# Performance work log

Hardware: AMD Instinct MI355X
Metric: run time of the kernel (lower is better)

The kernel has to match this reference:

```python
import jax, jax.numpy as jnp
import numpy as np

B, Hh, Ww = 8, 64, 64
D_MODEL, D_STATE, D_INNER = 96, 16, 192
R, DH, K = 6, 32, 4           # dt_rank, headdim, scan directions
KR = K * R                    # 24 heads
CHUNK = 64
LN_EPS = 1e-5


def setup_inputs() -> dict:
    key = jax.random.key(0)
    ks = jax.random.split(key, 8)
    s = 0.02
    return {
        "x": jax.random.normal(ks[0], (B, Hh, Ww, D_MODEL), jnp.float32),
        "in_proj_w": jax.random.normal(ks[1], (2 * D_INNER, D_MODEL), jnp.float32) * s,
        "conv_w": jax.random.normal(ks[2], (D_INNER, 1, 3, 3), jnp.float32) * s,
        "conv_b": jnp.zeros((D_INNER,), jnp.float32),
        "x_proj_w": jax.random.normal(ks[3], (K, R + 2 * D_STATE, D_INNER), jnp.float32) * s,
        "A_logs": jnp.zeros((K, R), jnp.float32),          # initialize='v2'
        "Ds": jnp.ones((K, R, DH), jnp.float32),
        "dt_bias": 0.1 * jax.random.uniform(ks[4], (K, R), jnp.float32),
        "ln_w": jnp.ones((D_INNER,), jnp.float32),
        "ln_b": jnp.zeros((D_INNER,), jnp.float32),
        "out_proj_w": jax.random.normal(ks[5], (D_MODEL, D_INNER), jnp.float32) * s,
    }


def _dwconv(x, w, b):
    # x: (B,H,W,C); torch weight (C,1,3,3) -> HWIO (3,3,1,C); depthwise conv, SAME pad
    kern = jnp.transpose(w, (2, 3, 1, 0))
    y = jax.lax.conv_general_dilated(
        x, kern, (1, 1), "SAME",
        dimension_numbers=("NHWC", "HWIO", "NHWC"),
        feature_group_count=x.shape[-1])
    return y + b


def _cross_scan(x):
    # x: (B,H,W,C) -> (B,L,4,C): row-major, col-major, and their reverses
    b, h, w, c = x.shape
    x0 = x.reshape(b, h * w, c)
    x1 = jnp.transpose(x, (0, 2, 1, 3)).reshape(b, h * w, c)
    return jnp.stack([x0, x1, x0[:, ::-1], x1[:, ::-1]], axis=2)


def _cross_merge(ys, h, w):
    # ys: (B,L,4,C) -> (B,L,C), inverse of _cross_scan, summed
    b, l, _, c = ys.shape
    y0 = ys[:, :, 0]
    y1 = jnp.transpose(ys[:, :, 1].reshape(b, w, h, c), (0, 2, 1, 3)).reshape(b, l, c)
    y2 = ys[:, ::-1, 2]
    y3 = jnp.transpose(ys[:, ::-1, 3].reshape(b, w, h, c), (0, 2, 1, 3)).reshape(b, l, c)
    return y0 + y1 + y2 + y3


def _chunk_scan(xs, dts, A, Bm, Cm, Dp, dtb):
    # Mamba2-style chunked selective scan.
    # xs: (B,L,KR,DH), dts: (B,L,KR), A: (KR,), Bm/Cm: (B,L,K,N), Dp: (KR,DH), dtb: (KR,)
    bq, l, h, dh = xs.shape
    n = Bm.shape[-1]
    q = CHUNK
    nc = l // q
    dt = jax.nn.softplus(dts + dtb)                       # (B,L,H)
    g = jnp.arange(h) // R                                # head -> group
    xr = xs.reshape(bq, nc, q, h, dh)
    dtr = dt.reshape(bq, nc, q, h)
    Brh = Bm.reshape(bq, nc, q, K, n)[:, :, :, g, :]      # (B,nc,Q,H,N)
    Crh = Cm.reshape(bq, nc, q, K, n)[:, :, :, g, :]
    dA = dtr * A                                          # (B,nc,Q,H), <= 0
    cum = jnp.cumsum(dA, axis=2)
    # intra-chunk attention-like term
    seg = cum[:, :, :, None, :] - cum[:, :, None, :, :]   # (B,nc,Qt,Qs,H)
    mask = jnp.tril(jnp.ones((q, q), bool))[None, None, :, :, None]
    Mw = jnp.where(mask, jnp.exp(seg), 0.0)
    CB = jnp.einsum("bcthn,bcshn->bctsh", Crh, Brh)
    Wt = CB * Mw * dtr[:, :, None, :, :]                  # dt at source step s
    y_intra = jnp.einsum("bctsh,bcshd->bcthd", Wt, xr)
    # per-chunk contribution to state and chunk decay
    decay_end = jnp.exp(cum[:, :, -1:, :] - cum)          # (B,nc,Q,H)
    S_loc = jnp.einsum("bcsh,bcshn,bcshd->bchdn", decay_end * dtr, Brh, xr)
    a_chunk = jnp.exp(cum[:, :, -1, :])                   # (B,nc,H)
    def step(state, inp):
        a, s = inp
        return a[:, :, None, None] * state + s, state     # emit state BEFORE chunk
    init = jnp.zeros((bq, h, dh, n), xs.dtype)
    _, prevs = jax.lax.scan(step, init, (jnp.moveaxis(a_chunk, 1, 0), jnp.moveaxis(S_loc, 1, 0)))
    prev_states = jnp.moveaxis(prevs, 0, 1)               # (B,nc,H,DH,N)
    y_inter = jnp.einsum("bcth,bcthn,bchdn->bcthd", jnp.exp(cum), Crh, prev_states)
    y = y_intra + y_inter + xr * Dp
    return y.reshape(bq, l, h, dh)


def _layernorm(x, w, b):
    mu = jnp.mean(x, -1, keepdims=True)
    var = jnp.mean(jnp.square(x - mu), -1, keepdims=True)
    return (x - mu) * jax.lax.rsqrt(var + LN_EPS) * w + b


def reference(x, in_proj_w, conv_w, conv_b, x_proj_w, A_logs, Ds, dt_bias, ln_w, ln_b, out_proj_w):
    bq, hh, ww, _ = x.shape
    l = hh * ww
    xz = x @ in_proj_w.T                                  # (B,H,W,2*Dinner)
    xh, z = jnp.split(xz, 2, axis=-1)
    z = jax.nn.silu(z)
    xh = jax.nn.silu(_dwconv(xh, conv_w, conv_b))
    xs = _cross_scan(xh)                                  # (B,L,K,Dinner)
    x_dbl = jnp.einsum("blkd,kcd->blkc", xs, x_proj_w)
    dts, Bs, Cs = jnp.split(x_dbl, [R, R + D_STATE], axis=3)
    xs = xs.reshape(bq, l, KR, DH)
    dts = dts.reshape(bq, l, KR)
    A = -jnp.exp(A_logs.reshape(KR))
    Dp = Ds.reshape(KR, DH)
    dtb = dt_bias.reshape(KR)
    ys = _chunk_scan(xs, dts, A, Bs, Cs, Dp, dtb)         # (B,L,KR,DH)
    y = _cross_merge(ys.reshape(bq, l, K, D_INNER), hh, ww)
    y = _layernorm(y, ln_w, ln_b).reshape(bq, hh, ww, D_INNER)
    y = y * z
    return y @ out_proj_w.T
```

## Files before the change

kernel.cpp:

```cpp
#include <hip/hip_runtime.h>
#include <hip/hip_bf16.h>

using bf16 = __hip_bfloat16;
typedef float f32;
typedef __attribute__((ext_vector_type(8))) short bf16x8;
typedef __attribute__((ext_vector_type(4))) float f32x4;
typedef __attribute__((ext_vector_type(4))) unsigned short u16x4;
typedef __attribute__((ext_vector_type(8))) unsigned short u16x8;

static __device__ __forceinline__ f32 siluf(f32 v){ return v / (1.f + __expf(-v)); }
static __device__ __forceinline__ unsigned short f2bf(f32 v){
  __hip_bfloat16 h=__float2bfloat16(v); return *(unsigned short*)&h;
}
static __device__ __forceinline__ f32 bfr2f(unsigned short u){
  unsigned int x=((unsigned int)u)<<16; return __uint_as_float(x);
}

static __device__ __forceinline__ int pos_of(int dir, int p){
  if(dir==0) return p;
  if(dir==1) return ((p&63)<<6) | (p>>6);
  if(dir==2) return 4095-p;
  int q = 4095-p; return ((q&63)<<6) | (q>>6);
}

static __device__ __forceinline__ f32 wave_iscan(f32 v, int lane){
  #pragma unroll
  for(int off=1; off<64; off<<=1){
    f32 u=__shfl_up(v,off,64);
    if(lane>=off) v+=u;
  }
  return v;
}
static __device__ __forceinline__ f32 wave_sscan(f32 v, int lane){
  #pragma unroll
  for(int off=1; off<64; off<<=1){
    f32 u=__shfl_down(v,off,64);
    if(lane<64-off) v+=u;
  }
  return v;
}

__global__ __launch_bounds__(256) void k_wcvt_all(const f32* __restrict__ xpw, const f32* __restrict__ ipw,
                                                  const f32* __restrict__ opw, const f32* __restrict__ dsw,
                                                  unsigned short* __restrict__ Wx, unsigned short* __restrict__ Wi,
                                                  unsigned short* __restrict__ Wo, f32* __restrict__ Dsum){
  const int t=blockIdx.x*256+threadIdx.x;
  if(t<3840){
    const int g=t%24, n=t/24, nt=n>>4, l=n&15;
    const int dir=n/40, cc=n-dir*40;
    u16x8 w={0,0,0,0,0,0,0,0};
    if(cc<38){
      const f32* p=&xpw[(size_t)dir*7296+cc*192+g*8];
      #pragma unroll
      for(int j=0;j<8;j++) w[j]=f2bf(p[j]);
    }
    *(u16x8*)&Wx[((size_t)(nt*24+g)*16+l)*8]=w;
  } else if(t<8448){
    const int i=t-3840, g=i%12, n=i/12, nt=n>>4, l=n&15;
    const f32* p=&ipw[(size_t)n*96+g*8];
    u16x8 w;
    #pragma unroll
    for(int j=0;j<8;j++) w[j]=f2bf(p[j]);
    *(u16x8*)&Wi[((size_t)(nt*12+g)*16+l)*8]=w;
  } else if(t<10752){
    const int i=t-8448, g=i%24, n=i/24, nt=n>>4, l=n&15;
    const f32* p=&opw[(size_t)n*192+g*8];
    u16x8 w;
    #pragma unroll
    for(int j=0;j<8;j++) w[j]=f2bf(p[j]);
    *(u16x8*)&Wo[((size_t)(nt*24+g)*16+l)*8]=w;
  } else if(t<10944){
    const int ch=t-10752;
    Dsum[ch]=dsw[ch]+dsw[192+ch]+dsw[384+ch]+dsw[576+ch];
  }
}

__global__ __launch_bounds__(256) void k_inproj(const f32* __restrict__ x, const unsigned short* __restrict__ Wi,
                                                f32* __restrict__ xh_raw, f32* __restrict__ z){
  __shared__ unsigned short Ald[12*64*8];
  const int m0=blockIdx.x*64, tid=threadIdx.x;
  for(int i=tid;i<768;i+=256){
    int r=i&63, g=i>>6;
    const f32* p=&x[(size_t)(m0+r)*96+g*8];
    float4 v0=*(const float4*)p, v1=*(const float4*)(p+4);
    u16x8 w={f2bf(v0.x),f2bf(v0.y),f2bf(v0.z),f2bf(v0.w),
             f2bf(v1.x),f2bf(v1.y),f2bf(v1.z),f2bf(v1.w)};
    *(u16x8*)&Ald[(size_t)(g*64+r)*8]=w;
  }
  __syncthreads();
  const int wv=tid>>6, lane=tid&63, l15=lane&15, l4=lane>>4;
  f32x4 acc[24];
  #pragma unroll
  for(int nt=0;nt<24;nt++){ f32x4 zz={0.f,0.f,0.f,0.f}; acc[nt]=zz; }
  #pragma unroll
  for(int ks=0;ks<3;ks++){
    const int g=ks*4+l4;
    bf16x8 a=*(const bf16x8*)&Ald[(size_t)(g*64+wv*16+l15)*8];
    #pragma unroll
    for(int nt=0;nt<24;nt++){
      bf16x8 bfr=*(const bf16x8*)&Wi[((size_t)(nt*12+g)*16+l15)*8];
      acc[nt]=__builtin_amdgcn_mfma_f32_16x16x32_bf16(a,bfr,acc[nt],0,0,0);
    }
  }
  const int rowb=m0+wv*16+l4*4;
  #pragma unroll
  for(int nt=0;nt<24;nt++){
    int col=nt*16+l15;
    #pragma unroll
    for(int r=0;r<4;r++){
      int row=rowb+r; f32 v=acc[nt][r];
      if(col<192) xh_raw[(size_t)row*192+col]=v;
      else        z[(size_t)row*192+(col-192)]=siluf(v);
    }
  }
}

__global__ __launch_bounds__(256) void k_conv(const f32* __restrict__ xh_raw, const f32* __restrict__ cw,
                                              const f32* __restrict__ cb, f32* __restrict__ xh){
  __shared__ f32 wsm[192][9];
  __shared__ f32 bsm[192];
  const int tid=threadIdx.x;
  for(int i=tid;i<1728;i+=256) wsm[i/9][i%9]=cw[i];
  for(int i=tid;i<192;i+=256) bsm[i]=cb[i];
  __syncthreads();
  const int idx=blockIdx.x*256+tid;
  const int c4=idx%48, j=(idx/48)&63, ii0=(idx/3072)&63, b=idx/196608;
  const int c0=c4*4;
  f32 acc[4]={bsm[c0],bsm[c0+1],bsm[c0+2],bsm[c0+3]};
  #pragma unroll
  for(int a=0;a<3;a++){
    int ii=ii0+a-1; if(ii<0||ii>63) continue;
    #pragma unroll
    for(int bb=0;bb<3;bb++){
      int jj=j+bb-1; if(jj<0||jj>63) continue;
      float4 v=*(const float4*)&xh_raw[((size_t)(b*4096)+(ii*64+jj))*192 + c0];
      int t=a*3+bb;
      acc[0]+=v.x*wsm[c0][t]; acc[1]+=v.y*wsm[c0+1][t];
      acc[2]+=v.z*wsm[c0+2][t]; acc[3]+=v.w*wsm[c0+3][t];
    }
  }
  float4 o; o.x=siluf(acc[0]); o.y=siluf(acc[1]); o.z=siluf(acc[2]); o.w=siluf(acc[3]);
  ((float4*)xh)[idx]=o;
}

__global__ __launch_bounds__(256) void k_xdbl(const f32* __restrict__ xh, const unsigned short* __restrict__ Wfrag,
                                              const f32* __restrict__ dtb, f32* __restrict__ dt_sp,
                                              f32* __restrict__ Bg, f32* __restrict__ Cg){
  __shared__ unsigned short Ald[24*64*8];
  const int m0=blockIdx.x*64;
  const int tid=threadIdx.x;
  for(int i=tid;i<1536;i+=256){
    int r=i&63, g=i>>6;
    const f32* p=&xh[(size_t)(m0+r)*192 + g*8];
    float4 v0=*(const float4*)p, v1=*(const float4*)(p+4);
    u16x8 w={f2bf(v0.x),f2bf(v0.y),f2bf(v0.z),f2bf(v0.w),
             f2bf(v1.x),f2bf(v1.y),f2bf(v1.z),f2bf(v1.w)};
    *(u16x8*)&Ald[(size_t)(g*64+r)*8]=w;
  }
  __syncthreads();
  const int wv=tid>>6, lane=tid&63, l15=lane&15, l4=lane>>4;
  f32x4 acc[10];
  #pragma unroll
  for(int nt=0;nt<10;nt++){ f32x4 zz={0.f,0.f,0.f,0.f}; acc[nt]=zz; }
  #pragma unroll
  for(int ks=0;ks<6;ks++){
    const int g=ks*4+l4;
    bf16x8 a=*(const bf16x8*)&Ald[(size_t)(g*64 + wv*16 + l15)*8];
    #pragma unroll
    for(int nt=0;nt<10;nt++){
      bf16x8 bfr=*(const bf16x8*)&Wfrag[((size_t)(nt*24+g)*16+l15)*8];
      acc[nt]=__builtin_amdgcn_mfma_f32_16x16x32_bf16(a,bfr,acc[nt],0,0,0);
    }
  }
  const int rowb=m0 + wv*16 + l4*4;
  #pragma unroll
  for(int nt=0;nt<10;nt++){
    int n=nt*16+l15, dir=n/40, cc=n-dir*40;
    if(cc>=38) continue;
    #pragma unroll
    for(int r=0;r<4;r++){
      size_t pix=(size_t)(rowb+r);
      f32 v=acc[nt][r];
      if(cc<6){ f32 xv=v+dtb[dir*6+cc]; dt_sp[pix*24+dir*6+cc]=(xv>20.f)? xv : log1pf(__expf(xv)); }
      else if(cc<22){ Bg[(pix*4+dir)*16+(cc-6)]=v; }
      else          { Cg[(pix*4+dir)*16+(cc-22)]=v; }
    }
  }
}

#define LDK1 72
__global__ __launch_bounds__(384) void k_chunk1(const f32* __restrict__ xh, const f32* __restrict__ Bg,
      const f32* __restrict__ dt_sp, const f32* __restrict__ Alogs, f32* __restrict__ S, f32* __restrict__ ach){
  __shared__ unsigned short Bp[192*LDK1];
  __shared__ unsigned short BtT[16*LDK1];
  __shared__ f32 dtl[64][6], w1l[64][6];
  __shared__ f32 e63[6];
  const int c=blockIdx.x, dir=blockIdx.y, b=blockIdx.z, c0=c*64, tid=threadIdx.x;
  { int r=tid/6, q=tid-r*6; size_t pix=(size_t)b*4096+pos_of(dir,c0+r);
    dtl[r][q]=dt_sp[pix*24+dir*6+q]; }
  if(tid<256){
    int r=tid>>2,q=tid&3; size_t pix=(size_t)b*4096+pos_of(dir,c0+r);
    float4 bv=*(const float4*)&Bg[(pix*4+dir)*16+q*4];
    BtT[(4*q+0)*LDK1+r]=f2bf(bv.x); BtT[(4*q+1)*LDK1+r]=f2bf(bv.y);
    BtT[(4*q+2)*LDK1+r]=f2bf(bv.z); BtT[(4*q+3)*LDK1+r]=f2bf(bv.w);
  }
  __syncthreads();
  const int wv=tid>>6, lane=tid&63;
  {
    f32 A=-__expf(Alogs[dir*6+wv]);
    f32 dv=dtl[lane][wv];
    f32 v=wave_iscan(dv*A,lane);
    w1l[lane][wv]=__expf(-v)*dv;
    if(lane==63){
      f32 e=__expf(v);
      e63[wv]=e;
      ach[((size_t)(b*64+c))*24+dir*6+wv]=e;
    }
  }
  __syncthreads();
  for(int u=tid;u<768;u+=384){
    int sg=u/48, q=u-sg*48, head=q>>3;
    f32 vv[4][4];
    #pragma unroll
    for(int j=0;j<4;j++){
      int s=sg*4+j;
      float4 xv=((const float4*)&xh[(size_t)(b*4096+pos_of(dir,c0+s))*192])[q];
      f32 w1=w1l[s][head];
      vv[j][0]=xv.x*w1; vv[j][1]=xv.y*w1; vv[j][2]=xv.z*w1; vv[j][3]=xv.w*w1;
    }
    #pragma unroll
    for(int cc=0;cc<4;cc++){
      u16x4 w={f2bf(vv[0][cc]),f2bf(vv[1][cc]),f2bf(vv[2][cc]),f2bf(vv[3][cc])};
      *(u16x4*)&Bp[(4*q+cc)*LDK1+sg*4]=w;
    }
  }
  __syncthreads();
  const int l15=lane&15, l4=lane>>4;
  f32x4 acc[2];
  { f32x4 zz={0.f,0.f,0.f,0.f}; acc[0]=zz; acc[1]=zz; }
  #pragma unroll
  for(int i=0;i<2;i++){
    int mt=wv+6*i;
    #pragma unroll
    for(int ks=0;ks<2;ks++){
      int kg=ks*4+l4;
      bf16x8 a=*(const bf16x8*)&Bp[(size_t)(mt*16+l15)*LDK1+kg*8];
      bf16x8 bb=*(const bf16x8*)&BtT[(size_t)l15*LDK1+kg*8];
      acc[i]=__builtin_amdgcn_mfma_f32_16x16x32_bf16(a,bb,acc[i],0,0,0);
    }
  }
  const size_t base=(((size_t)(b*64+c))*24+dir*6)*512;
  #pragma unroll
  for(int i=0;i<2;i++){
    int mt=wv+6*i;
    #pragma unroll
    for(int r=0;r<4;r++){
      int ch=mt*16+l4*4+r, head=ch>>5, d=ch&31;
      S[base+(size_t)head*512+d*16+l15]=acc[i][r]*e63[head];
    }
  }
}

__global__ __launch_bounds__(256) void k_scan(f32* __restrict__ S, const f32* __restrict__ ach){
  const int g=blockIdx.x*256+threadIdx.x;
  const int b=g/12288, rem=g%12288, h=rem/512;
  size_t base=(size_t)b*786432 + rem;
  const f32* ap=&ach[(size_t)b*1536 + h];
  f32 st=0.f;
  for(int c=0;c<64;c++){
    f32 a=ap[c*24];
    f32 s=S[base+(size_t)c*12288];
    S[base+(size_t)c*12288]=st;
    st=a*st+s;
  }
}

#define LDK 104
__global__ __launch_bounds__(384) void k_chunk2(const f32* __restrict__ xh, const f32* __restrict__ Bg,
      const f32* __restrict__ Cg, const f32* __restrict__ dt_sp, const f32* __restrict__ Sprev,
      const f32* __restrict__ Alogs,
      f32* __restrict__ ym0, f32* __restrict__ ym1){
  __shared__ unsigned short Alds[64*LDK];
  __shared__ unsigned short Blds[96*LDK];
  __shared__ unsigned short Btf[64*32];
  __shared__ f32 w1l[64][6], erowl[64][6];
  const int c=blockIdx.x, b=blockIdx.y, pair=blockIdx.z>>1, half=blockIdx.z&1;
  const int c0=c*64, tid=threadIdx.x;
  f32* __restrict__ ym = pair? ym1 : ym0;
  const int wv=tid>>6, lane=tid&63, l15=lane&15, l4=lane>>4;
  f32 vsum[4][4];
  #pragma unroll
  for(int mt=0;mt<4;mt++){
    #pragma unroll
    for(int r=0;r<4;r++) vsum[mt][r]=0.f;
  }
  const int gch=half*96+wv*16+l15, ohead=gch>>5;
  #pragma unroll
  for(int d=0;d<2;d++){
    const int dir=pair+d*2;
    const int cd=d? (63-c) : c;
    if(d) __syncthreads();
    if(tid<256){
      int r=tid>>2,q=tid&3;
      size_t pix=(size_t)b*4096 + (pair==0 ? (c0+r) : (r*64+c));
      float4 bv=*(const float4*)&Bg[(pix*4+dir)*16+q*4];
      float4 cv=*(const float4*)&Cg[(pix*4+dir)*16+q*4];
      u16x4 wb={f2bf(bv.x),f2bf(bv.y),f2bf(bv.z),f2bf(bv.w)};
      u16x4 wc={f2bf(cv.x),f2bf(cv.y),f2bf(cv.z),f2bf(cv.w)};
      u16x4 zz={0,0,0,0};
      *(u16x4*)&Btf[r*32+q*4]=wb;      *(u16x4*)&Btf[r*32+16+q*4]=zz;
      *(u16x4*)&Alds[r*LDK+64+q*4]=wc; *(u16x4*)&Alds[r*LDK+80+q*4]=zz;
    }
    {
      const size_t pbase=(((size_t)(b*64+cd))*24+dir*6)*512;
      int lr=tid>>2, ng=tid&3, g2=half*96+lr, hh=g2>>5, dd=g2&31;
      float4 pv=*(const float4*)&Sprev[pbase+(size_t)hh*512+dd*16+ng*4];
      u16x4 w={f2bf(pv.x),f2bf(pv.y),f2bf(pv.z),f2bf(pv.w)};
      u16x4 zz={0,0,0,0};
      *(u16x4*)&Blds[lr*LDK+64+ng*4]=w;
      *(u16x4*)&Blds[lr*LDK+80+ng*4]=zz;
    }
    {
      f32 Aa=-__expf(Alogs[dir*6+wv]);
      size_t pixL=(size_t)b*4096 + (pair==0 ? (c0+lane) : (lane*64+c));
      f32 dv=dt_sp[pixL*24+dir*6+wv];
      f32 sc = d? wave_sscan(dv*Aa,lane) : wave_iscan(dv*Aa,lane);
      w1l[lane][wv]=__expf(-sc)*dv;
      erowl[lane][wv]=__expf(sc);
    }
    __syncthreads();
    #pragma unroll
    for(int tt=0;tt<3;tt++){
      int tile=wv+6*tt;
      if(tile<16){
        int mt=tile>>2, nt=tile&3;
        f32x4 a4={0.f,0.f,0.f,0.f};
        bf16x8 af=*(const bf16x8*)&Alds[(mt*16+l15)*LDK+64+l4*8];
        bf16x8 bfr=*(const bf16x8*)&Btf[(nt*16+l15)*32+l4*8];
        a4=__builtin_amdgcn_mfma_f32_16x16x32_bf16(af,bfr,a4,0,0,0);
        #pragma unroll
        for(int r=0;r<4;r++){
          int t=mt*16+l4*4+r, s=nt*16+l15;
          bool keep = d? (s>=t) : (s<=t);
          Alds[t*LDK+s]= keep? f2bf(a4[r]) : (unsigned short)0;
        }
      }
    }
    {
      int sg=tid/24, ql=tid-sg*24;
      int head=(half*96+ql*4)>>5;
      f32 vv[4][4];
      #pragma unroll
      for(int j=0;j<4;j++){
        int s=sg*4+j;
        size_t pix=(size_t)b*4096 + (pair==0 ? (c0+s) : (s*64+c));
        float4 xv=*(const float4*)&xh[pix*192 + half*96 + ql*4];
        f32 w1=w1l[s][head];
        vv[j][0]=xv.x*w1; vv[j][1]=xv.y*w1; vv[j][2]=xv.z*w1; vv[j][3]=xv.w*w1;
      }
      #pragma unroll
      for(int cc=0;cc<4;cc++){
        u16x4 w={f2bf(vv[0][cc]),f2bf(vv[1][cc]),f2bf(vv[2][cc]),f2bf(vv[3][cc])};
        *(u16x4*)&Blds[(4*ql+cc)*LDK+sg*4]=w;
      }
    }
    __syncthreads();
    f32x4 acc[4];
    #pragma unroll
    for(int mt=0;mt<4;mt++){ f32x4 zz={0.f,0.f,0.f,0.f}; acc[mt]=zz; }
    #pragma unroll
    for(int ks=0;ks<3;ks++){
      const int kg=ks*4+l4;
      bf16x8 bfr=*(const bf16x8*)&Blds[(wv*16+l15)*LDK+kg*8];
      #pragma unroll
      for(int mt=0;mt<4;mt++){
        bf16x8 af=*(const bf16x8*)&Alds[(mt*16+l15)*LDK+kg*8];
        acc[mt]=__builtin_amdgcn_mfma_f32_16x16x32_bf16(af,bfr,acc[mt],0,0,0);
      }
    }
    #pragma unroll
    for(int mt=0;mt<4;mt++){
      #pragma unroll
      for(int r=0;r<4;r++){
        int t=mt*16+l4*4+r;
        vsum[mt][r]+=acc[mt][r]*erowl[t][ohead];
      }
    }
  }
  #pragma unroll
  for(int mt=0;mt<4;mt++){
    #pragma unroll
    for(int r=0;r<4;r++){
      int t=mt*16+l4*4+r;
      size_t pix=(size_t)b*4096 + (pair==0 ? (c0+t) : (t*64+c));
      ym[pix*192+gch]=vsum[mt][r];
    }
  }
}

__global__ __launch_bounds__(256) void k_outproj(const f32* __restrict__ ym0, const f32* __restrict__ ym1,
                                                 const f32* __restrict__ xh, const f32* __restrict__ Dsum,
                                                 const f32* __restrict__ z,
                                                 const f32* __restrict__ lw, const f32* __restrict__ lb,
                                                 const unsigned short* __restrict__ Wo, f32* __restrict__ out){
  __shared__ unsigned short Ald[24*64*8];
  __shared__ f32 lws[192], lbs[192], dss[192];
  const int m0=blockIdx.x*64, tid=threadIdx.x;
  for(int i=tid;i<192;i+=256){ lws[i]=lw[i]; lbs[i]=lb[i]; dss[i]=Dsum[i]; }
  __syncthreads();
  const int r=tid>>2, sub=tid&3;
  const size_t base=(size_t)(m0+r)*192 + sub*48;
  f32 y[48];
  f32 s=0.f;
  #pragma unroll
  for(int j=0;j<48;j+=4){
    float4 a=*(const float4*)&ym0[base+j];
    float4 bb=*(const float4*)&ym1[base+j];
    float4 xv=*(const float4*)&xh[base+j];
    int col=sub*48+j;
    y[j]  =a.x+bb.x+xv.x*dss[col];
    y[j+1]=a.y+bb.y+xv.y*dss[col+1];
    y[j+2]=a.z+bb.z+xv.z*dss[col+2];
    y[j+3]=a.w+bb.w+xv.w*dss[col+3];
    s+=y[j]+y[j+1]+y[j+2]+y[j+3];
  }
  s+=__shfl_xor(s,1,64); s+=__shfl_xor(s,2,64);
  const f32 mu=s*(1.f/192.f);
  f32 q=0.f;
  #pragma unroll
  for(int j=0;j<48;j++){ f32 dd=y[j]-mu; q+=dd*dd; }
  q+=__shfl_xor(q,1,64); q+=__shfl_xor(q,2,64);
  const f32 rs=rsqrtf(q*(1.f/192.f)+1e-5f);
  #pragma unroll
  for(int j=0;j<48;j+=8){
    float4 z0=*(const float4*)&z[base+j];
    float4 z1=*(const float4*)&z[base+j+4];
    int col=sub*48+j;
    u16x8 w;
    w[0]=f2bf(((y[j+0]-mu)*rs*lws[col+0]+lbs[col+0])*z0.x);
    w[1]=f2bf(((y[j+1]-mu)*rs*lws[col+1]+lbs[col+1])*z0.y);
    w[2]=f2bf(((y[j+2]-mu)*rs*lws[col+2]+lbs[col+2])*z0.z);
    w[3]=f2bf(((y[j+3]-mu)*rs*lws[col+3]+lbs[col+3])*z0.w);
    w[4]=f2bf(((y[j+4]-mu)*rs*lws[col+4]+lbs[col+4])*z1.x);
    w[5]=f2bf(((y[j+5]-mu)*rs*lws[col+5]+lbs[col+5])*z1.y);
    w[6]=f2bf(((y[j+6]-mu)*rs*lws[col+6]+lbs[col+6])*z1.z);
    w[7]=f2bf(((y[j+7]-mu)*rs*lws[col+7]+lbs[col+7])*z1.w);
    int g=col>>3;
    *(u16x8*)&Ald[((size_t)g*64+r)*8]=w;
  }
  __syncthreads();
  const int wv=tid>>6, lane=tid&63, l15=lane&15, l4=lane>>4;
  f32x4 acc[6];
  #pragma unroll
  for(int nt=0;nt<6;nt++){ f32x4 zz={0.f,0.f,0.f,0.f}; acc[nt]=zz; }
  #pragma unroll
  for(int ks=0;ks<6;ks++){
    const int g=ks*4+l4;
    bf16x8 a=*(const bf16x8*)&Ald[(size_t)(g*64+wv*16+l15)*8];
    #pragma unroll
    for(int nt=0;nt<6;nt++){
      bf16x8 bfr=*(const bf16x8*)&Wo[((size_t)(nt*24+g)*16+l15)*8];
      acc[nt]=__builtin_amdgcn_mfma_f32_16x16x32_bf16(a,bfr,acc[nt],0,0,0);
    }
  }
  const int rowb=m0+wv*16+l4*4;
  #pragma unroll
  for(int nt=0;nt<6;nt++){
    int col=nt*16+l15;
    #pragma unroll
    for(int r2=0;r2<4;r2++){
      out[(size_t)(rowb+r2)*96+col]=acc[nt][r2];
    }
  }
}

extern "C" void kernel_launch(void* const* d_in, const int* in_sizes, int n_in,
                              void* d_out, int out_size, void* d_ws, size_t ws_size,
                              hipStream_t stream){
  const f32* x  =(const f32*)d_in[0];
  const f32* ipw=(const f32*)d_in[1];
  const f32* cw =(const f32*)d_in[2];
  const f32* cb =(const f32*)d_in[3];
  const f32* xpw=(const f32*)d_in[4];
  const f32* alg=(const f32*)d_in[5];
  const f32* dsw=(const f32*)d_in[6];
  const f32* dtb=(const f32*)d_in[7];
  const f32* lw =(const f32*)d_in[8];
  const f32* lb =(const f32*)d_in[9];
  const f32* opw=(const f32*)d_in[10];
  f32* out=(f32*)d_out;
  f32* ws=(f32*)d_ws;

  f32* xh_raw=ws;
  f32* z     =ws+ 6291456;
  f32* xh    =ws+12582912;
  f32* dt_sp =ws+18874368;
  f32* Bg    =ws+19660800;
  f32* Cg    =ws+21757952;
  f32* S     =ws+23855104;
  f32* ach   =ws+30146560;
  f32* ym1   =ws+30158848;
  unsigned short* Wx=(unsigned short*)(ws+36450304);
  unsigned short* Wi=(unsigned short*)(ws+36465664);
  unsigned short* Wo=(unsigned short*)(ws+36484096);
  f32* Dsum  =ws+36493312;
  f32* ym0=xh_raw;

  k_wcvt_all<<<43,256,0,stream>>>(xpw,ipw,opw,dsw,Wx,Wi,Wo,Dsum);
  k_inproj<<<512,256,0,stream>>>(x,Wi,xh_raw,z);
  k_conv<<<6144,256,0,stream>>>(xh_raw,cw,cb,xh);
  k_xdbl<<<dim3(512),256,0,stream>>>(xh,Wx,dtb,dt_sp,Bg,Cg);
  k_chunk1<<<dim3(64,4,8),384,0,stream>>>(xh,Bg,dt_sp,alg,S,ach);
  k_scan<<<384,256,0,stream>>>(S,ach);
  k_chunk2<<<dim3(64,8,4),384,0,stream>>>(xh,Bg,Cg,dt_sp,S,alg,ym0,ym1);
  k_outproj<<<512,256,0,stream>>>(ym0,ym1,xh,Dsum,z,lw,lb,Wo,out);
}
```

Measured before the change: 189.1 us.

## Fuse depthwise conv into x_dbl projection and merge chunk2 channel halves

The depthwise 3x3 conv + SiLU is folded into the x_dbl projection kernel. Each block computes the conv for its 64 pixels, writes xh for later stages and feeds bf16 tiles straight into shared memory, so one launch and a full re-read of xh are removed. k_chunk2 now uses 768-thread blocks that cover all 192 channels instead of two 96-channel halves. The dt cumulative scans for both directions are hoisted out of the loop, and the intra-chunk C·B matrix and B/C loads are no longer duplicated across halves. The trade-off is more shared memory and fewer, larger blocks, which can lower occupancy, and the fused conv reloads neighbour pixels through global/L2 without sharing them via LDS.

```diff
diff --git a/kernel.cpp b/kernel.cpp
--- a/kernel.cpp
+++ b/kernel.cpp
@@ -115,46 +115,45 @@
   }
 }
 
-__global__ __launch_bounds__(256) void k_conv(const f32* __restrict__ xh_raw, const f32* __restrict__ cw,
-                                              const f32* __restrict__ cb, f32* __restrict__ xh){
-  __shared__ f32 wsm[192][9];
+__global__ __launch_bounds__(256) void k_xdblconv(const f32* __restrict__ xh_raw, const f32* __restrict__ cw,
+                                              const f32* __restrict__ cb, const unsigned short* __restrict__ Wfrag,
+                                              const f32* __restrict__ dtb, f32* __restrict__ xh,
+                                              f32* __restrict__ dt_sp, f32* __restrict__ Bg, f32* __restrict__ Cg){
+  __shared__ unsigned short Ald[24*64*8];
+  __shared__ f32 wsm[9][200];
   __shared__ f32 bsm[192];
-  const int tid=threadIdx.x;
-  for(int i=tid;i<1728;i+=256) wsm[i/9][i%9]=cw[i];
+  const int blk=blockIdx.x, m0=blk*64, tid=threadIdx.x;
+  const int b=blk>>6, irow=blk&63;
+  for(int i=tid;i<1728;i+=256){ int ch=i/9, t=i-ch*9; wsm[t][ch]=cw[i]; }
   for(int i=tid;i<192;i+=256) bsm[i]=cb[i];
   __syncthreads();
-  const int idx=blockIdx.x*256+tid;
-  const int c4=idx%48, j=(idx/48)&63, ii0=(idx/3072)&63, b=idx/196608;
-  const int c0=c4*4;
-  f32 acc[4]={bsm[c0],bsm[c0+1],bsm[c0+2],bsm[c0+3]};
-  #pragma unroll
-  for(int a=0;a<3;a++){
-    int ii=ii0+a-1; if(ii<0||ii>63) continue;
-    #pragma unroll
-    for(int bb=0;bb<3;bb++){
-      int jj=j+bb-1; if(jj<0||jj>63) continue;
-      float4 v=*(const float4*)&xh_raw[((size_t)(b*4096)+(ii*64+jj))*192 + c0];
-      int t=a*3+bb;
-      acc[0]+=v.x*wsm[c0][t]; acc[1]+=v.y*wsm[c0+1][t];
-      acc[2]+=v.z*wsm[c0+2][t]; acc[3]+=v.w*wsm[c0+3][t];
-    }
-  }
-  float4 o; o.x=siluf(acc[0]); o.y=siluf(acc[1]); o.z=siluf(acc[2]); o.w=siluf(acc[3]);
-  ((float4*)xh)[idx]=o;
-}
-
-__global__ __launch_bounds__(256) void k_xdbl(const f32* __restrict__ xh, const unsigned short* __restrict__ Wfrag,
-                                              const f32* __restrict__ dtb, f32* __restrict__ dt_sp,
-                                              f32* __restrict__ Bg, f32* __restrict__ Cg){
-  __shared__ unsigned short Ald[24*64*8];
-  const int m0=blockIdx.x*64;
-  const int tid=threadIdx.x;
   for(int i=tid;i<1536;i+=256){
     int r=i&63, g=i>>6;
-    const f32* p=&xh[(size_t)(m0+r)*192 + g*8];
-    float4 v0=*(const float4*)p, v1=*(const float4*)(p+4);
-    u16x8 w={f2bf(v0.x),f2bf(v0.y),f2bf(v0.z),f2bf(v0.w),
-             f2bf(v1.x),f2bf(v1.y),f2bf(v1.z),f2bf(v1.w)};
+    f32 acc[8];
+    #pragma unroll
+    for(int k=0;k<8;k++) acc[k]=bsm[g*8+k];
+    #pragma unroll
+    for(int a=0;a<3;a++){
+      int ii=irow+a-1; if(ii<0||ii>63) continue;
+      #pragma unroll
+      for(int bb=0;bb<3;bb++){
+        int jj=r+bb-1; if(jj<0||jj>63) continue;
+        const f32* p=&xh_raw[((size_t)(b*4096)+(ii*64+jj))*192+g*8];
+        float4 v0=*(const float4*)p, v1=*(const float4*)(p+4);
+        int t=a*3+bb;
+        acc[0]+=v0.x*wsm[t][g*8+0]; acc[1]+=v0.y*wsm[t][g*8+1];
+        acc[2]+=v0.z*wsm[t][g*8+2]; acc[3]+=v0.w*wsm[t][g*8+3];
+        acc[4]+=v1.x*wsm[t][g*8+4]; acc[5]+=v1.y*wsm[t][g*8+5];
+        acc[6]+=v1.z*wsm[t][g*8+6]; acc[7]+=v1.w*wsm[t][g*8+7];
+      }
+    }
+    f32 o[8];
+    u16x8 w;
+    #pragma unroll
+    for(int k=0;k<8;k++){ o[k]=siluf(acc[k]); w[k]=f2bf(o[k]); }
+    f32* op=&xh[(size_t)(m0+r)*192+g*8];
+    float4 o0={o[0],o[1],o[2],o[3]}, o1={o[4],o[5],o[6],o[7]};
+    *(float4*)op=o0; *(float4*)(op+4)=o1;
     *(u16x8*)&Ald[(size_t)(g*64+r)*8]=w;
   }
   __syncthreads();
@@ -276,25 +275,35 @@
 }
 
 #define LDK 104
-__global__ __launch_bounds__(384) void k_chunk2(const f32* __restrict__ xh, const f32* __restrict__ Bg,
+__global__ __launch_bounds__(768) void k_chunk2(const f32* __restrict__ xh, const f32* __restrict__ Bg,
       const f32* __restrict__ Cg, const f32* __restrict__ dt_sp, const f32* __restrict__ Sprev,
       const f32* __restrict__ Alogs,
       f32* __restrict__ ym0, f32* __restrict__ ym1){
   __shared__ unsigned short Alds[64*LDK];
-  __shared__ unsigned short Blds[96*LDK];
+  __shared__ unsigned short Blds[192*LDK];
   __shared__ unsigned short Btf[64*32];
-  __shared__ f32 w1l[64][6], erowl[64][6];
-  const int c=blockIdx.x, b=blockIdx.y, pair=blockIdx.z>>1, half=blockIdx.z&1;
+  __shared__ f32 w1l[2][64][6], erowl[2][64][6];
+  const int c=blockIdx.x, b=blockIdx.y, pair=blockIdx.z;
   const int c0=c*64, tid=threadIdx.x;
   f32* __restrict__ ym = pair? ym1 : ym0;
   const int wv=tid>>6, lane=tid&63, l15=lane&15, l4=lane>>4;
+  {
+    int ds=(wv>=6)?1:0, head=ds? wv-6 : wv;
+    int dirs=pair+2*ds;
+    f32 Aa=-__expf(Alogs[dirs*6+head]);
+    size_t pixL=(size_t)b*4096 + (pair==0 ? (c0+lane) : (lane*64+c));
+    f32 dv=dt_sp[pixL*24+dirs*6+head];
+    f32 sc = ds? wave_sscan(dv*Aa,lane) : wave_iscan(dv*Aa,lane);
+    w1l[ds][lane][head]=__expf(-sc)*dv;
+    erowl[ds][lane][head]=__expf(sc);
+  }
   f32 vsum[4][4];
   #pragma unroll
   for(int mt=0;mt<4;mt++){
     #pragma unroll
     for(int r=0;r<4;r++) vsum[mt][r]=0.f;
   }
-  const int gch=half*96+wv*16+l15, ohead=gch>>5;
+  const int gch=wv*16+l15, ohead=gch>>5;
   #pragma unroll
   for(int d=0;d<2;d++){
     const int dir=pair+d*2;
@@ -313,25 +322,17 @@
     }
     {
       const size_t pbase=(((size_t)(b*64+cd))*24+dir*6)*512;
-      int lr=tid>>2, ng=tid&3, g2=half*96+lr, hh=g2>>5, dd=g2&31;
+      int lr=tid>>2, ng=tid&3, hh=lr>>5, dd=lr&31;
       float4 pv=*(const float4*)&Sprev[pbase+(size_t)hh*512+dd*16+ng*4];
       u16x4 w={f2bf(pv.x),f2bf(pv.y),f2bf(pv.z),f2bf(pv.w)};
       u16x4 zz={0,0,0,0};
       *(u16x4*)&Blds[lr*LDK+64+ng*4]=w;
       *(u16x4*)&Blds[lr*LDK+80+ng*4]=zz;
     }
-    {
-      f32 Aa=-__expf(Alogs[dir*6+wv]);
-      size_t pixL=(size_t)b*4096 + (pair==0 ? (c0+lane) : (lane*64+c));
-      f32 dv=dt_sp[pixL*24+dir*6+wv];
-      f32 sc = d? wave_sscan(dv*Aa,lane) : wave_iscan(dv*Aa,lane);
-      w1l[lane][wv]=__expf(-sc)*dv;
-      erowl[lane][wv]=__expf(sc);
-    }
     __syncthreads();
     #pragma unroll
-    for(int tt=0;tt<3;tt++){
-      int tile=wv+6*tt;
+    for(int tt=0;tt<2;tt++){
+      int tile=wv+12*tt;
       if(tile<16){
         int mt=tile>>2, nt=tile&3;
         f32x4 a4={0.f,0.f,0.f,0.f};
@@ -347,21 +348,21 @@
       }
     }
     {
-      int sg=tid/24, ql=tid-sg*24;
-      int head=(half*96+ql*4)>>5;
+      int sg=tid/48, q=tid-sg*48;
+      int head=q>>3;
       f32 vv[4][4];
       #pragma unroll
       for(int j=0;j<4;j++){
         int s=sg*4+j;
         size_t pix=(size_t)b*4096 + (pair==0 ? (c0+s) : (s*64+c));
-        float4 xv=*(const float4*)&xh[pix*192 + half*96 + ql*4];
-        f32 w1=w1l[s][head];
+        float4 xv=*(const float4*)&xh[pix*192 + q*4];
+        f32 w1=w1l[d][s][head];
         vv[j][0]=xv.x*w1; vv[j][1]=xv.y*w1; vv[j][2]=xv.z*w1; vv[j][3]=xv.w*w1;
       }
       #pragma unroll
       for(int cc=0;cc<4;cc++){
         u16x4 w={f2bf(vv[0][cc]),f2bf(vv[1][cc]),f2bf(vv[2][cc]),f2bf(vv[3][cc])};
-        *(u16x4*)&Blds[(4*ql+cc)*LDK+sg*4]=w;
+        *(u16x4*)&Blds[(4*q+cc)*LDK+sg*4]=w;
       }
     }
     __syncthreads();
@@ -383,7 +384,7 @@
       #pragma unroll
       for(int r=0;r<4;r++){
         int t=mt*16+l4*4+r;
-        vsum[mt][r]+=acc[mt][r]*erowl[t][ohead];
+        vsum[mt][r]+=acc[mt][r]*erowl[d][t][ohead];
       }
     }
   }
@@ -508,10 +509,9 @@
 
   k_wcvt_all<<<43,256,0,stream>>>(xpw,ipw,opw,dsw,Wx,Wi,Wo,Dsum);
   k_inproj<<<512,256,0,stream>>>(x,Wi,xh_raw,z);
-  k_conv<<<6144,256,0,stream>>>(xh_raw,cw,cb,xh);
-  k_xdbl<<<dim3(512),256,0,stream>>>(xh,Wx,dtb,dt_sp,Bg,Cg);
+  k_xdblconv<<<512,256,0,stream>>>(xh_raw,cw,cb,Wx,dtb,xh,dt_sp,Bg,Cg);
   k_chunk1<<<dim3(64,4,8),384,0,stream>>>(xh,Bg,dt_sp,alg,S,ach);
   k_scan<<<384,256,0,stream>>>(S,ach);
-  k_chunk2<<<dim3(64,8,4),384,0,stream>>>(xh,Bg,Cg,dt_sp,S,alg,ym0,ym1);
+  k_chunk2<<<dim3(64,8,2),768,0,stream>>>(xh,Bg,Cg,dt_sp,S,alg,ym0,ym1);
   k_outproj<<<512,256,0,stream>>>(ym0,ym1,xh,Dsum,z,lw,lb,Wo,out);
 }
```

Measured after the change: 188.0 us. About the same (-0.6%).

## Halve GEMM row tiles and merge chunk2 channel halves into one 768-thread block

Applied to the files above, without the earlier changes.

k_inproj and k_xdbl now process 32 rows per block instead of 64, with the four waves split over two M-tiles and two N-halves. This doubles the grid and cuts per-thread accumulator registers. k_chunk2 drops the two-way channel split: each block now handles all 192 channels with 768 threads, so the C/B intra-chunk matrix and Bt fragments are built once rather than twice per chunk. The decay scans for both directions are also computed up front. The trade-off is larger LDS use and bigger blocks in chunk2, which may lower occupancy.

```diff
diff --git a/kernel.cpp b/kernel.cpp
--- a/kernel.cpp
+++ b/kernel.cpp
@@ -77,38 +77,39 @@
 
 __global__ __launch_bounds__(256) void k_inproj(const f32* __restrict__ x, const unsigned short* __restrict__ Wi,
                                                 f32* __restrict__ xh_raw, f32* __restrict__ z){
-  __shared__ unsigned short Ald[12*64*8];
-  const int m0=blockIdx.x*64, tid=threadIdx.x;
-  for(int i=tid;i<768;i+=256){
-    int r=i&63, g=i>>6;
+  __shared__ unsigned short Ald[12*32*8];
+  const int m0=blockIdx.x*32, tid=threadIdx.x;
+  for(int i=tid;i<384;i+=256){
+    int r=i&31, g=i>>5;
     const f32* p=&x[(size_t)(m0+r)*96+g*8];
     float4 v0=*(const float4*)p, v1=*(const float4*)(p+4);
     u16x8 w={f2bf(v0.x),f2bf(v0.y),f2bf(v0.z),f2bf(v0.w),
              f2bf(v1.x),f2bf(v1.y),f2bf(v1.z),f2bf(v1.w)};
-    *(u16x8*)&Ald[(size_t)(g*64+r)*8]=w;
+    *(u16x8*)&Ald[(size_t)(g*32+r)*8]=w;
   }
   __syncthreads();
   const int wv=tid>>6, lane=tid&63, l15=lane&15, l4=lane>>4;
-  f32x4 acc[24];
-  #pragma unroll
-  for(int nt=0;nt<24;nt++){ f32x4 zz={0.f,0.f,0.f,0.f}; acc[nt]=zz; }
+  const int mt=wv&1, ntb=(wv>>1)*12;
+  f32x4 acc[12];
+  #pragma unroll
+  for(int j=0;j<12;j++){ f32x4 zz={0.f,0.f,0.f,0.f}; acc[j]=zz; }
   #pragma unroll
   for(int ks=0;ks<3;ks++){
     const int g=ks*4+l4;
-    bf16x8 a=*(const bf16x8*)&Ald[(size_t)(g*64+wv*16+l15)*8];
-    #pragma unroll
-    for(int nt=0;nt<24;nt++){
-      bf16x8 bfr=*(const bf16x8*)&Wi[((size_t)(nt*12+g)*16+l15)*8];
-      acc[nt]=__builtin_amdgcn_mfma_f32_16x16x32_bf16(a,bfr,acc[nt],0,0,0);
-    }
-  }
-  const int rowb=m0+wv*16+l4*4;
-  #pragma unroll
-  for(int nt=0;nt<24;nt++){
-    int col=nt*16+l15;
+    bf16x8 a=*(const bf16x8*)&Ald[(size_t)(g*32+mt*16+l15)*8];
+    #pragma unroll
+    for(int j=0;j<12;j++){
+      bf16x8 bfr=*(const bf16x8*)&Wi[((size_t)((ntb+j)*12+g)*16+l15)*8];
+      acc[j]=__builtin_amdgcn_mfma_f32_16x16x32_bf16(a,bfr,acc[j],0,0,0);
+    }
+  }
+  const int rowb=m0+mt*16+l4*4;
+  #pragma unroll
+  for(int j=0;j<12;j++){
+    int col=(ntb+j)*16+l15;
     #pragma unroll
     for(int r=0;r<4;r++){
-      int row=rowb+r; f32 v=acc[nt][r];
+      int row=rowb+r; f32 v=acc[j][r];
       if(col<192) xh_raw[(size_t)row*192+col]=v;
       else        z[(size_t)row*192+(col-192)]=siluf(v);
     }
@@ -146,41 +147,42 @@
 __global__ __launch_bounds__(256) void k_xdbl(const f32* __restrict__ xh, const unsigned short* __restrict__ Wfrag,
                                               const f32* __restrict__ dtb, f32* __restrict__ dt_sp,
                                               f32* __restrict__ Bg, f32* __restrict__ Cg){
-  __shared__ unsigned short Ald[24*64*8];
-  const int m0=blockIdx.x*64;
+  __shared__ unsigned short Ald[24*32*8];
+  const int m0=blockIdx.x*32;
   const int tid=threadIdx.x;
-  for(int i=tid;i<1536;i+=256){
-    int r=i&63, g=i>>6;
+  for(int i=tid;i<768;i+=256){
+    int r=i&31, g=i>>5;
     const f32* p=&xh[(size_t)(m0+r)*192 + g*8];
     float4 v0=*(const float4*)p, v1=*(const float4*)(p+4);
     u16x8 w={f2bf(v0.x),f2bf(v0.y),f2bf(v0.z),f2bf(v0.w),
              f2bf(v1.x),f2bf(v1.y),f2bf(v1.z),f2bf(v1.w)};
-    *(u16x8*)&Ald[(size_t)(g*64+r)*8]=w;
+    *(u16x8*)&Ald[(size_t)(g*32+r)*8]=w;
   }
   __syncthreads();
   const int wv=tid>>6, lane=tid&63, l15=lane&15, l4=lane>>4;
-  f32x4 acc[10];
-  #pragma unroll
-  for(int nt=0;nt<10;nt++){ f32x4 zz={0.f,0.f,0.f,0.f}; acc[nt]=zz; }
+  const int mt=wv&1, ntb=(wv>>1)*5;
+  f32x4 acc[5];
+  #pragma unroll
+  for(int j=0;j<5;j++){ f32x4 zz={0.f,0.f,0.f,0.f}; acc[j]=zz; }
   #pragma unroll
   for(int ks=0;ks<6;ks++){
     const int g=ks*4+l4;
-    bf16x8 a=*(const bf16x8*)&Ald[(size_t)(g*64 + wv*16 + l15)*8];
-    #pragma unroll
-    for(int nt=0;nt<10;nt++){
-      bf16x8 bfr=*(const bf16x8*)&Wfrag[((size_t)(nt*24+g)*16+l15)*8];
-      acc[nt]=__builtin_amdgcn_mfma_f32_16x16x32_bf16(a,bfr,acc[nt],0,0,0);
-    }
-  }
-  const int rowb=m0 + wv*16 + l4*4;
-  #pragma unroll
-  for(int nt=0;nt<10;nt++){
-    int n=nt*16+l15, dir=n/40, cc=n-dir*40;
+    bf16x8 a=*(const bf16x8*)&Ald[(size_t)(g*32 + mt*16 + l15)*8];
+    #pragma unroll
+    for(int j=0;j<5;j++){
+      bf16x8 bfr=*(const bf16x8*)&Wfrag[((size_t)((ntb+j)*24+g)*16+l15)*8];
+      acc[j]=__builtin_amdgcn_mfma_f32_16x16x32_bf16(a,bfr,acc[j],0,0,0);
+    }
+  }
+  const int rowb=m0 + mt*16 + l4*4;
+  #pragma unroll
+  for(int j=0;j<5;j++){
+    int n=(ntb+j)*16+l15, dir=n/40, cc=n-dir*40;
     if(cc>=38) continue;
     #pragma unroll
     for(int r=0;r<4;r++){
       size_t pix=(size_t)(rowb+r);
-      f32 v=acc[nt][r];
+      f32 v=acc[j][r];
       if(cc<6){ f32 xv=v+dtb[dir*6+cc]; dt_sp[pix*24+dir*6+cc]=(xv>20.f)? xv : log1pf(__expf(xv)); }
       else if(cc<22){ Bg[(pix*4+dir)*16+(cc-6)]=v; }
       else          { Cg[(pix*4+dir)*16+(cc-22)]=v; }
@@ -276,25 +278,35 @@
 }
 
 #define LDK 104
-__global__ __launch_bounds__(384) void k_chunk2(const f32* __restrict__ xh, const f32* __restrict__ Bg,
+__global__ __launch_bounds__(768) void k_chunk2(const f32* __restrict__ xh, const f32* __restrict__ Bg,
       const f32* __restrict__ Cg, const f32* __restrict__ dt_sp, const f32* __restrict__ Sprev,
       const f32* __restrict__ Alogs,
       f32* __restrict__ ym0, f32* __restrict__ ym1){
   __shared__ unsigned short Alds[64*LDK];
-  __shared__ unsigned short Blds[96*LDK];
+  __shared__ unsigned short Blds[192*LDK];
   __shared__ unsigned short Btf[64*32];
-  __shared__ f32 w1l[64][6], erowl[64][6];
-  const int c=blockIdx.x, b=blockIdx.y, pair=blockIdx.z>>1, half=blockIdx.z&1;
+  __shared__ f32 w1l[2][64][6], erowl[2][64][6];
+  const int c=blockIdx.x, b=blockIdx.y, pair=blockIdx.z;
   const int c0=c*64, tid=threadIdx.x;
   f32* __restrict__ ym = pair? ym1 : ym0;
   const int wv=tid>>6, lane=tid&63, l15=lane&15, l4=lane>>4;
+  {
+    int ds=(wv>=6)?1:0, head=ds? wv-6 : wv;
+    int dirs=pair+2*ds;
+    f32 Aa=-__expf(Alogs[dirs*6+head]);
+    size_t pixL=(size_t)b*4096 + (pair==0 ? (c0+lane) : (lane*64+c));
+    f32 dv=dt_sp[pixL*24+dirs*6+head];
+    f32 sc = ds? wave_sscan(dv*Aa,lane) : wave_iscan(dv*Aa,lane);
+    w1l[ds][lane][head]=__expf(-sc)*dv;
+    erowl[ds][lane][head]=__expf(sc);
+  }
   f32 vsum[4][4];
   #pragma unroll
   for(int mt=0;mt<4;mt++){
     #pragma unroll
     for(int r=0;r<4;r++) vsum[mt][r]=0.f;
   }
-  const int gch=half*96+wv*16+l15, ohead=gch>>5;
+  const int gch=wv*16+l15, ohead=gch>>5;
   #pragma unroll
   for(int d=0;d<2;d++){
     const int dir=pair+d*2;
@@ -313,25 +325,17 @@
     }
     {
       const size_t pbase=(((size_t)(b*64+cd))*24+dir*6)*512;
-      int lr=tid>>2, ng=tid&3, g2=half*96+lr, hh=g2>>5, dd=g2&31;
+      int lr=tid>>2, ng=tid&3, hh=lr>>5, dd=lr&31;
       float4 pv=*(const float4*)&Sprev[pbase+(size_t)hh*512+dd*16+ng*4];
       u16x4 w={f2bf(pv.x),f2bf(pv.y),f2bf(pv.z),f2bf(pv.w)};
       u16x4 zz={0,0,0,0};
       *(u16x4*)&Blds[lr*LDK+64+ng*4]=w;
       *(u16x4*)&Blds[lr*LDK+80+ng*4]=zz;
     }
-    {
-      f32 Aa=-__expf(Alogs[dir*6+wv]);
-      size_t pixL=(size_t)b*4096 + (pair==0 ? (c0+lane) : (lane*64+c));
-      f32 dv=dt_sp[pixL*24+dir*6+wv];
-      f32 sc = d? wave_sscan(dv*Aa,lane) : wave_iscan(dv*Aa,lane);
-      w1l[lane][wv]=__expf(-sc)*dv;
-      erowl[lane][wv]=__expf(sc);
-    }
     __syncthreads();
     #pragma unroll
-    for(int tt=0;tt<3;tt++){
-      int tile=wv+6*tt;
+    for(int tt=0;tt<2;tt++){
+      int tile=wv+12*tt;
       if(tile<16){
         int mt=tile>>2, nt=tile&3;
         f32x4 a4={0.f,0.f,0.f,0.f};
@@ -347,21 +351,21 @@
       }
     }
     {
-      int sg=tid/24, ql=tid-sg*24;
-      int head=(half*96+ql*4)>>5;
+      int sg=tid/48, q=tid-sg*48;
+      int head=q>>3;
       f32 vv[4][4];
       #pragma unroll
       for(int j=0;j<4;j++){
         int s=sg*4+j;
         size_t pix=(size_t)b*4096 + (pair==0 ? (c0+s) : (s*64+c));
-        float4 xv=*(const float4*)&xh[pix*192 + half*96 + ql*4];
-        f32 w1=w1l[s][head];
+        float4 xv=*(const float4*)&xh[pix*192 + q*4];
+        f32 w1=w1l[d][s][head];
         vv[j][0]=xv.x*w1; vv[j][1]=xv.y*w1; vv[j][2]=xv.z*w1; vv[j][3]=xv.w*w1;
       }
       #pragma unroll
       for(int cc=0;cc<4;cc++){
         u16x4 w={f2bf(vv[0][cc]),f2bf(vv[1][cc]),f2bf(vv[2][cc]),f2bf(vv[3][cc])};
-        *(u16x4*)&Blds[(4*ql+cc)*LDK+sg*4]=w;
+        *(u16x4*)&Blds[(4*q+cc)*LDK+sg*4]=w;
       }
     }
     __syncthreads();
@@ -383,7 +387,7 @@
       #pragma unroll
       for(int r=0;r<4;r++){
         int t=mt*16+l4*4+r;
-        vsum[mt][r]+=acc[mt][r]*erowl[t][ohead];
+        vsum[mt][r]+=acc[mt][r]*erowl[d][t][ohead];
       }
     }
   }
@@ -507,11 +511,11 @@
   f32* ym0=xh_raw;
 
   k_wcvt_all<<<43,256,0,stream>>>(xpw,ipw,opw,dsw,Wx,Wi,Wo,Dsum);
-  k_inproj<<<512,256,0,stream>>>(x,Wi,xh_raw,z);
+  k_inproj<<<1024,256,0,stream>>>(x,Wi,xh_raw,z);
   k_conv<<<6144,256,0,stream>>>(xh_raw,cw,cb,xh);
-  k_xdbl<<<dim3(512),256,0,stream>>>(xh,Wx,dtb,dt_sp,Bg,Cg);
+  k_xdbl<<<1024,256,0,stream>>>(xh,Wx,dtb,dt_sp,Bg,Cg);
   k_chunk1<<<dim3(64,4,8),384,0,stream>>>(xh,Bg,dt_sp,alg,S,ach);
   k_scan<<<384,256,0,stream>>>(S,ach);
-  k_chunk2<<<dim3(64,8,4),384,0,stream>>>(xh,Bg,Cg,dt_sp,S,alg,ym0,ym1);
+  k_chunk2<<<dim3(64,8,2),768,0,stream>>>(xh,Bg,Cg,dt_sp,S,alg,ym0,ym1);
   k_outproj<<<512,256,0,stream>>>(ym0,ym1,xh,Dsum,z,lw,lb,Wo,out);
 }
```

After: 178.9 us. -5.4%, faster.
